# Kernel optimization log

Hardware: AMD Instinct MI355X
Metric: run time of the kernel (lower is better)

Reference implementation:

```python
import jax, jax.numpy as jnp
import numpy as np

BETA = 2
KERAS_EPS = 1e-7  # keras.backend.epsilon()


def _masks(n):
    idx = np.arange(n)
    # eps2[i,j] = 1 iff i<j  (itertools.combinations for N=2)
    eps2 = (idx[:, None] < idx[None, :]).astype(np.float32)
    # eps3[i,j,k] = 1 iff i<j<k  (itertools.combinations for N=3)
    eps3 = ((idx[:, None, None] < idx[None, :, None])
            & (idx[None, :, None] < idx[None, None, :])).astype(np.float32)
    return jnp.asarray(eps2), jnp.asarray(eps3)


def _jet_ecf(x, beta):
    # x: [B, n, 3] = (pt, eta, phi)
    n = x.shape[1]
    pt = x[:, :, 0]    # [B, n]
    eta = x[:, :, 1]
    phi = x[:, :, 2]
    # pairwise squared distance in (eta, phi): [B, n, n]
    R2 = (eta[:, :, None] - eta[:, None, :]) ** 2 \
       + (phi[:, :, None] - phi[:, None, :]) ** 2
    if beta == 2:
        Rb = R2
    elif beta == 1:
        Rb = jnp.sqrt(R2)
    else:
        Rb = R2 ** (beta / 2)

    eps2, eps3 = _masks(n)

    ecf1 = jnp.sum(pt, axis=-1, keepdims=True)                         # [B, 1]
    ecf2 = jnp.einsum('ij,ai,aj,aij->a', eps2, pt, pt, Rb)[:, None]    # [B, 1]
    ecf3 = jnp.einsum('ijk,ai,aj,ak,aij,aik,ajk->a',
                      eps3, pt, pt, pt, Rb, Rb, Rb)[:, None]           # [B, 1]
    return ecf1, ecf2, ecf3


def setup_inputs() -> dict:
    key = jax.random.key(0)
    x = jax.random.normal(key, (2048, 200, 3), dtype=jnp.float32)
    return {"x": x}


def reference(x):
    ecf1, ecf2, ecf3 = _jet_ecf(x, BETA)
    d2 = ecf3 * ecf1 ** 3 / (ecf2 ** 3 + KERAS_EPS)
    return jnp.concatenate([ecf1, ecf2, ecf3, d2], axis=-1)  # [B, 4]
```

## Files before the change

kernel.cpp:

```cpp
#include <hip/hip_runtime.h>


constexpr int NPART = 200;
typedef float f2 __attribute__((ext_vector_type(2)));

__device__ __forceinline__ float bcast(float v, int ii) {
    return __int_as_float(__builtin_amdgcn_readlane(__float_as_int(v), ii));
}

constexpr int offA(int g) {
    return (g < 72) ? g : (g == 135 ? 135 : g - 64);
}

struct Ctx {
    f2 bw[5], be[5], bp[5];
    f2 acc23, accY, tt;
    f2 pe01, pp01, pe23, pp23, pe13, pp13, n1;
    float a0, a1, a2, a3;
    float pe1, pp1, pe3, pp3;
    unsigned aw, ae, ap;
    int lane;
};

template <int G>
__device__ __forceinline__ void prefetch(Ctx& c) {
    constexpr int A = offA(G), B = G, S = G % 5;
    asm volatile(
        "ds_read2_b32 %[w], %[aw] offset0:%c[A] offset1:%c[B]\n\t"
        "ds_read2_b32 %[e], %[ae] offset0:%c[A] offset1:%c[B]\n\t"
        "ds_read2_b32 %[p], %[ap] offset0:%c[A] offset1:%c[B]\n\t"
        : [w] "+v"(c.bw[S]), [e] "+v"(c.be[S]), [p] "+v"(c.bp[S])
        : [aw] "v"(c.aw), [ae] "v"(c.ae), [ap] "v"(c.ap), [A] "i"(A), [B] "i"(B));
}

template <int G>
__device__ __forceinline__ void cstep(Ctx& c) {
    constexpr int rem = 198 - G;
    constexpr int K = 3 * (rem < 4 ? rem : 4);
    constexpr int S = G % 5;
    if constexpr (G <= 6) {
        f2 t1, t2;
        asm volatile(
            "s_waitcnt lgkmcnt(%c[K])\n\t"
            "v_pk_fma_f32 %[t1], %[pe01], %[n1], %[be]\n\t"
            "v_pk_fma_f32 %[t2], %[pp01], %[n1], %[bp]\n\t"
            "v_pk_mul_f32 %[t1], %[t1], %[t1]\n\t"
            "v_pk_mul_f32 %[t2], %[t2], %[t2]\n\t"
            "v_pk_add_f32 %[t1], %[t1], %[t2]\n\t"
            "v_pk_mul_f32 %[tt], %[t1], %[bw]\n\t"
            "v_pk_fma_f32 %[t1], %[pe23], %[n1], %[be]\n\t"
            "v_pk_fma_f32 %[t2], %[pp23], %[n1], %[bp]\n\t"
            "v_pk_mul_f32 %[t1], %[t1], %[t1]\n\t"
            "v_pk_mul_f32 %[t2], %[t2], %[t2]\n\t"
            "v_pk_add_f32 %[t1], %[t1], %[t2]\n\t"
            "v_pk_mul_f32 %[t1], %[t1], %[bw]\n\t"
            "v_pk_add_f32 %[acc], %[acc], %[t1]\n\t"
            : [t1] "=&v"(t1), [t2] "=&v"(t2), [tt] "=&v"(c.tt),
              [acc] "+v"(c.acc23), [bw] "+v"(c.bw[S]), [be] "+v"(c.be[S]),
              [bp] "+v"(c.bp[S])
            : [pe01] "v"(c.pe01), [pp01] "v"(c.pp01), [pe23] "v"(c.pe23),
              [pp23] "v"(c.pp23), [n1] "v"(c.n1), [K] "i"(K));
        c.a1 = __fadd_rn(c.a1, c.tt.y);
        c.a0 = __fadd_rn(c.a0, (G < c.lane) ? c.tt.x : 0.0f);
    } else if constexpr (G <= 71) {
        f2 t1, t2;
        asm volatile(
            "s_waitcnt lgkmcnt(%c[K])\n\t"
            "v_pk_fma_f32 %[t1], %[pe23], %[n1], %[be]\n\t"
            "v_pk_fma_f32 %[t2], %[pp23], %[n1], %[bp]\n\t"
            "v_pk_mul_f32 %[t1], %[t1], %[t1]\n\t"
            "v_pk_mul_f32 %[t2], %[t2], %[t2]\n\t"
            "v_pk_add_f32 %[t1], %[t1], %[t2]\n\t"
            "v_pk_mul_f32 %[t1], %[t1], %[bw]\n\t"
            "v_pk_add_f32 %[acc], %[acc], %[t1]\n\t"
            : [t1] "=&v"(t1), [t2] "=&v"(t2), [acc] "+v"(c.acc23),
              [bw] "+v"(c.bw[S]), [be] "+v"(c.be[S]), [bp] "+v"(c.bp[S])
            : [pe23] "v"(c.pe23), [pp23] "v"(c.pp23), [n1] "v"(c.n1), [K] "i"(K));
        if constexpr (G == 7) {
            const float de = __fsub_rn(c.be[S].x, c.pe1);
            const float dp = __fsub_rn(c.bp[S].x, c.pp1);
            const float r2 = __fadd_rn(__fmul_rn(de, de), __fmul_rn(dp, dp));
            c.a1 = __fadd_rn(c.a1, __fmul_rn(r2, c.bw[S].x));
        }
    } else if constexpr (G <= 134) {
        if constexpr (G == 72) { c.a2 = c.acc23.x; c.a3 = c.acc23.y; }
        f2 t1, t2;
        asm volatile(
            "s_waitcnt lgkmcnt(%c[K])\n\t"
            "v_pk_fma_f32 %[t1], %[pe13], %[n1], %[be]\n\t"
            "v_pk_fma_f32 %[t2], %[pp13], %[n1], %[bp]\n\t"
            "v_pk_mul_f32 %[t1], %[t1], %[t1]\n\t"
            "v_pk_mul_f32 %[t2], %[t2], %[t2]\n\t"
            "v_pk_add_f32 %[t1], %[t1], %[t2]\n\t"
            "v_pk_mul_f32 %[tt], %[t1], %[bw]\n\t"
            : [t1] "=&v"(t1), [t2] "=&v"(t2), [tt] "=&v"(c.tt),
              [bw] "+v"(c.bw[S]), [be] "+v"(c.be[S]), [bp] "+v"(c.bp[S])
            : [pe13] "v"(c.pe13), [pp13] "v"(c.pp13), [n1] "v"(c.n1), [K] "i"(K));
        c.a3 = __fadd_rn(c.a3, c.tt.y);
        c.a1 = __fadd_rn(c.a1, ((G - 72) < c.lane) ? c.tt.x : 0.0f);
    } else if constexpr (G == 135) {
        asm volatile("s_waitcnt lgkmcnt(%c[K])"
                     : [bw] "+v"(c.bw[S]), [be] "+v"(c.be[S]), [bp] "+v"(c.bp[S])
                     : [K] "i"(K));
        const float de = __fsub_rn(c.be[S].x, c.pe3);
        const float dp = __fsub_rn(c.bp[S].x, c.pp3);
        const float r2 = __fadd_rn(__fmul_rn(de, de), __fmul_rn(dp, dp));
        c.a3 = __fadd_rn(c.a3, __fmul_rn(r2, c.bw[S].x));
    } else {
        if constexpr (G == 136) { c.accY.x = c.a2; c.accY.y = c.a3; }
        constexpr unsigned sh = G - 135;
        constexpr unsigned lm = sh < 32 ? (0xFFFFFFFFu << sh) : 0u;
        constexpr unsigned hm = sh < 32 ? 0xFFFFFFFFu : (0xFFFFFFFFu << (sh - 32));
        f2 t1, t2;
        asm volatile(
            "s_waitcnt lgkmcnt(%c[K])\n\t"
            "s_mov_b32 exec_lo, %c[LM]\n\t"
            "s_mov_b32 exec_hi, %c[HM]\n\t"
            "v_pk_fma_f32 %[t1], %[pe23], %[n1], %[be]\n\t"
            "v_pk_fma_f32 %[t2], %[pp23], %[n1], %[bp]\n\t"
            "v_pk_mul_f32 %[t1], %[t1], %[t1]\n\t"
            "v_pk_mul_f32 %[t2], %[t2], %[t2]\n\t"
            "v_pk_add_f32 %[t1], %[t1], %[t2]\n\t"
            "v_pk_mul_f32 %[t1], %[t1], %[bw]\n\t"
            "v_pk_add_f32 %[acc], %[acc], %[t1]\n\t"
            "s_mov_b64 exec, -1\n\t"
            : [t1] "=&v"(t1), [t2] "=&v"(t2), [acc] "+v"(c.accY),
              [bw] "+v"(c.bw[S]), [be] "+v"(c.be[S]), [bp] "+v"(c.bp[S])
            : [pe23] "v"(c.pe23), [pp23] "v"(c.pp23), [n1] "v"(c.n1),
              [K] "i"(K), [LM] "i"(lm), [HM] "i"(hm));
    }
}

template <int G>
__device__ __forceinline__ void run(Ctx& c) {
    if constexpr (G <= 198) {
        cstep<G>(c);
        if constexpr (G + 5 <= 198) prefetch<G + 5>(c);
        run<G + 1>(c);
    }
}

__global__ __launch_bounds__(64) void jet_ecf_kernel(const float* __restrict__ x,
                                                     float* __restrict__ out,
                                                     int njet) {
#pragma clang fp contract(off)
    const int jet = blockIdx.x;
    if (jet >= njet) return;
    const int lane = threadIdx.x;
    const float* xj = x + (size_t)jet * NPART * 3;

    __shared__ float lds[600];

    float pw[4], pea[4], ppa[4];
    {
        const int base[4] = {0, 8, 72, 136};
        #pragma unroll
        for (int k = 0; k < 4; ++k) {
            const int p = base[k] + lane;
            const bool valid = (k > 0) || (lane < 8);
            if (valid) {
                pw[k] = xj[p * 3 + 0];
                pea[k] = xj[p * 3 + 1];
                ppa[k] = xj[p * 3 + 2];
            } else {
                pw[k] = 0.0f; pea[k] = 0.0f; ppa[k] = 0.0f;
            }
        }
    }

    #pragma unroll
    for (int r = 0; r < 4; ++r) {
        const int i = lane + (r << 6);
        if (i < NPART) {
            lds[i]       = xj[3 * i + 0];
            lds[200 + i] = xj[3 * i + 1];
            lds[400 + i] = xj[3 * i + 2];
        }
    }

    double S = 0, Sa = 0, Se = 0, Sp = 0, Saa = 0;
    double Sae = 0, Sap = 0, See = 0, Spp = 0, Sep = 0;
    #pragma unroll
    for (int k = 0; k < 4; ++k) {
        const double w = (double)pw[k];
        const double e = (double)pea[k];
        const double f = (double)ppa[k];
        const double a = e * e + f * f;
        S   += w;        Sa  += w * a;     Se  += w * e;
        Sp  += w * f;    Saa += w * a * a; Sae += w * a * e;
        Sap += w * a * f; See += w * e * e; Spp += w * f * f;
        Sep += w * e * f;
    }
    #pragma unroll
    for (int off = 32; off > 0; off >>= 1) {
        S   += __shfl_down(S,   off, 64);
        Sa  += __shfl_down(Sa,  off, 64);
        Se  += __shfl_down(Se,  off, 64);
        Sp  += __shfl_down(Sp,  off, 64);
        Saa += __shfl_down(Saa, off, 64);
        Sae += __shfl_down(Sae, off, 64);
        Sap += __shfl_down(Sap, off, 64);
        See += __shfl_down(See, off, 64);
        Spp += __shfl_down(Spp, off, 64);
        Sep += __shfl_down(Sep, off, 64);
    }

    __syncthreads();
    asm volatile("" ::: "memory");
    asm volatile("" :: "v"(S), "v"(Sa), "v"(Se), "v"(Sp), "v"(Saa),
                       "v"(Sae), "v"(Sap), "v"(See), "v"(Spp), "v"(Sep));
    __builtin_amdgcn_sched_barrier(0);
    asm volatile("s_waitcnt lgkmcnt(0)" ::: );

    Ctx c;
    c.lane = lane;
    c.aw = (unsigned)(uintptr_t)&lds[0];
    c.ae = (unsigned)(uintptr_t)&lds[200];
    c.ap = (unsigned)(uintptr_t)&lds[400];
    c.n1.x = -1.0f; c.n1.y = -1.0f;
    c.pe01.x = pea[0]; c.pe01.y = pea[1];
    c.pp01.x = ppa[0]; c.pp01.y = ppa[1];
    c.pe23.x = pea[2]; c.pe23.y = pea[3];
    c.pp23.x = ppa[2]; c.pp23.y = ppa[3];
    c.pe13.x = pea[1]; c.pe13.y = pea[3];
    c.pp13.x = ppa[1]; c.pp13.y = ppa[3];
    c.pe1 = pea[1]; c.pp1 = ppa[1]; c.pe3 = pea[3]; c.pp3 = ppa[3];
    c.acc23.x = 0.0f; c.acc23.y = 0.0f;
    c.accY.x = 0.0f;  c.accY.y = 0.0f;
    c.tt.x = 0.0f;    c.tt.y = 0.0f;
    c.a0 = c.a1 = c.a2 = c.a3 = 0.0f;
    #pragma unroll
    for (int k = 0; k < 5; ++k) {
        c.bw[k].x = 0.0f; c.bw[k].y = 0.0f;
        c.be[k].x = 0.0f; c.be[k].y = 0.0f;
        c.bp[k].x = 0.0f; c.bp[k].y = 0.0f;
    }

    prefetch<0>(c); prefetch<1>(c); prefetch<2>(c); prefetch<3>(c); prefetch<4>(c);
    run<0>(c);
    c.a2 = c.accY.x; c.a3 = c.accY.y;

    const float t0 = __fmul_rn(pw[0], c.a0);
    const float t1 = __fmul_rn(pw[1], c.a1);
    const float t2 = __fmul_rn(pw[2], c.a2);
    const float t3 = __fmul_rn(pw[3], c.a3);

    float e2f = 0.0f;
    #pragma unroll
    for (int ii = 0; ii < 8; ++ii)  e2f = __fadd_rn(e2f, bcast(t0, ii));
    #pragma unroll 8
    for (int ii = 0; ii < 64; ++ii) e2f = __fadd_rn(e2f, bcast(t1, ii));
    #pragma unroll 8
    for (int ii = 0; ii < 64; ++ii) e2f = __fadd_rn(e2f, bcast(t2, ii));
    #pragma unroll 8
    for (int ii = 0; ii < 64; ++ii) e2f = __fadd_rn(e2f, bcast(t3, ii));

    if (lane == 0) {
        const double A[4][4] = {
            {  Saa,        Sa,       -2.0 * Sae, -2.0 * Sap },
            {  Sa,         S,        -2.0 * Se,  -2.0 * Sp  },
            { -2.0 * Sae, -2.0 * Se,  4.0 * See,  4.0 * Sep },
            { -2.0 * Sap, -2.0 * Sp,  4.0 * Sep,  4.0 * Spp }
        };
        const double B[4][4] = {
            { Sa,  S,  -2.0 * Se,  -2.0 * Sp  },
            { Saa, Sa, -2.0 * Sae, -2.0 * Sap },
            { Sae, Se, -2.0 * See, -2.0 * Sep },
            { Sap, Sp, -2.0 * Sep, -2.0 * Spp }
        };
        const double C[4][4] = {
            { S,  Sa,  Se,  Sp  },
            { Sa, Saa, Sae, Sap },
            { Se, Sae, See, Sep },
            { Sp, Sap, Sep, Spp }
        };
        double T = 0.0;
        #pragma unroll
        for (int b = 0; b < 4; ++b) {
            #pragma unroll
            for (int g = 0; g < 4; ++g) {
                double ab = 0.0;
                #pragma unroll
                for (int al = 0; al < 4; ++al) ab += A[al][b] * B[al][g];
                T += ab * C[b][g];
            }
        }
        const double ecf1 = S;
        const double ecf2 = (double)e2f;
        const double ecf3 = T * (1.0 / 6.0);
        const double d2 = ecf3 * ecf1 * ecf1 * ecf1 / (ecf2 * ecf2 * ecf2 + 1e-7);
        float4 o = make_float4((float)ecf1, (float)ecf2, (float)ecf3, (float)d2);
        *reinterpret_cast<float4*>(out + (size_t)jet * 4) = o;
    }
}

extern "C" void kernel_launch(void* const* d_in, const int* in_sizes, int n_in,
                              void* d_out, int out_size, void* d_ws, size_t ws_size,
                              hipStream_t stream) {
    const float* x = (const float*)d_in[0];
    float* out = (float*)d_out;
    const int njet = in_sizes[0] / (NPART * 3);
    jet_ecf_kernel<<<njet, 64, 0, stream>>>(x, out, njet);
}
```

Baseline: 70.69 us.

## Replace readlane broadcast reduction with LDS staging and pack middle-phase accumulators

The final serial sum of 200 per-particle terms no longer uses 200 v_readlane broadcasts. Each term is written into a second shared array, partly early inside the main loop, and then read back as float4 vectors, keeping the sequential float add order. The middle phase now accumulates both outputs in one packed register pair with a cndmask lane mask instead of separate scalar adds. The moment sums use explicit double FMAs. The inline asm hardcodes v40-v43 and vcc as clobbers, and the LDS writes and reads are ordered only by a manual lgkmcnt wait with no barrier.

```diff
diff --git a/kernel.cpp b/kernel.cpp
--- a/kernel.cpp
+++ b/kernel.cpp
@@ -4,20 +4,18 @@
 constexpr int NPART = 200;
 typedef float f2 __attribute__((ext_vector_type(2)));
 
-__device__ __forceinline__ float bcast(float v, int ii) {
-    return __int_as_float(__builtin_amdgcn_readlane(__float_as_int(v), ii));
-}
-
 constexpr int offA(int g) {
     return (g < 72) ? g : (g == 135 ? 135 : g - 64);
 }
 
 struct Ctx {
     f2 bw[5], be[5], bp[5];
-    f2 acc23, accY, tt;
+    f2 acc23, accY, accM, tt;
     f2 pe01, pp01, pe23, pp23, pe13, pp13, n1;
-    float a0, a1, a2, a3;
+    float a0, a1;
     float pe1, pp1, pe3, pp3;
+    float pw0, pw1;
+    float* l2;
     unsigned aw, ae, ap;
     int lane;
 };
@@ -83,21 +81,23 @@
             c.a1 = __fadd_rn(c.a1, __fmul_rn(r2, c.bw[S].x));
         }
     } else if constexpr (G <= 134) {
-        if constexpr (G == 72) { c.a2 = c.acc23.x; c.a3 = c.acc23.y; }
-        f2 t1, t2;
+        if constexpr (G == 72) { c.accM.x = c.a1; c.accM.y = c.acc23.y; }
         asm volatile(
             "s_waitcnt lgkmcnt(%c[K])\n\t"
-            "v_pk_fma_f32 %[t1], %[pe13], %[n1], %[be]\n\t"
-            "v_pk_fma_f32 %[t2], %[pp13], %[n1], %[bp]\n\t"
-            "v_pk_mul_f32 %[t1], %[t1], %[t1]\n\t"
-            "v_pk_mul_f32 %[t2], %[t2], %[t2]\n\t"
-            "v_pk_add_f32 %[t1], %[t1], %[t2]\n\t"
-            "v_pk_mul_f32 %[tt], %[t1], %[bw]\n\t"
-            : [t1] "=&v"(t1), [t2] "=&v"(t2), [tt] "=&v"(c.tt),
-              [bw] "+v"(c.bw[S]), [be] "+v"(c.be[S]), [bp] "+v"(c.bp[S])
-            : [pe13] "v"(c.pe13), [pp13] "v"(c.pp13), [n1] "v"(c.n1), [K] "i"(K));
-        c.a3 = __fadd_rn(c.a3, c.tt.y);
-        c.a1 = __fadd_rn(c.a1, ((G - 72) < c.lane) ? c.tt.x : 0.0f);
+            "v_pk_fma_f32 v[40:41], %[pe13], %[n1], %[be]\n\t"
+            "v_pk_fma_f32 v[42:43], %[pp13], %[n1], %[bp]\n\t"
+            "v_pk_mul_f32 v[40:41], v[40:41], v[40:41]\n\t"
+            "v_pk_mul_f32 v[42:43], v[42:43], v[42:43]\n\t"
+            "v_pk_add_f32 v[40:41], v[40:41], v[42:43]\n\t"
+            "v_pk_mul_f32 v[40:41], v[40:41], %[bw]\n\t"
+            "v_cmp_lt_u32 vcc, %c[II], %[lane]\n\t"
+            "v_cndmask_b32 v40, 0, v40, vcc\n\t"
+            "v_pk_add_f32 %[acc], %[acc], v[40:41]\n\t"
+            : [acc] "+v"(c.accM), [bw] "+v"(c.bw[S]), [be] "+v"(c.be[S]),
+              [bp] "+v"(c.bp[S])
+            : [pe13] "v"(c.pe13), [pp13] "v"(c.pp13), [n1] "v"(c.n1),
+              [K] "i"(K), [II] "i"(G - 72), [lane] "v"(c.lane)
+            : "v40", "v41", "v42", "v43", "vcc");
     } else if constexpr (G == 135) {
         asm volatile("s_waitcnt lgkmcnt(%c[K])"
                      : [bw] "+v"(c.bw[S]), [be] "+v"(c.be[S]), [bp] "+v"(c.bp[S])
@@ -105,9 +105,9 @@
         const float de = __fsub_rn(c.be[S].x, c.pe3);
         const float dp = __fsub_rn(c.bp[S].x, c.pp3);
         const float r2 = __fadd_rn(__fmul_rn(de, de), __fmul_rn(dp, dp));
-        c.a3 = __fadd_rn(c.a3, __fmul_rn(r2, c.bw[S].x));
+        c.accM.y = __fadd_rn(c.accM.y, __fmul_rn(r2, c.bw[S].x));
     } else {
-        if constexpr (G == 136) { c.accY.x = c.a2; c.accY.y = c.a3; }
+        if constexpr (G == 136) { c.accY.x = c.acc23.x; c.accY.y = c.accM.y; }
         constexpr unsigned sh = G - 135;
         constexpr unsigned lm = sh < 32 ? (0xFFFFFFFFu << sh) : 0u;
         constexpr unsigned hm = sh < 32 ? 0xFFFFFFFFu : (0xFFFFFFFFu << (sh - 32));
@@ -135,6 +135,12 @@
 __device__ __forceinline__ void run(Ctx& c) {
     if constexpr (G <= 198) {
         cstep<G>(c);
+        if constexpr (G == 6) {
+            c.l2[c.lane] = __fmul_rn(c.pw0, c.a0);
+        }
+        if constexpr (G == 134) {
+            c.l2[8 + c.lane] = __fmul_rn(c.pw1, c.accM.x);
+        }
         if constexpr (G + 5 <= 198) prefetch<G + 5>(c);
         run<G + 1>(c);
     }
@@ -150,6 +156,7 @@
     const float* xj = x + (size_t)jet * NPART * 3;
 
     __shared__ float lds[600];
+    __shared__ __align__(16) float lds2[200];
 
     float pw[4], pea[4], ppa[4];
     {
@@ -185,11 +192,15 @@
         const double w = (double)pw[k];
         const double e = (double)pea[k];
         const double f = (double)ppa[k];
-        const double a = e * e + f * f;
-        S   += w;        Sa  += w * a;     Se  += w * e;
-        Sp  += w * f;    Saa += w * a * a; Sae += w * a * e;
-        Sap += w * a * f; See += w * e * e; Spp += w * f * f;
-        Sep += w * e * f;
+        const double a = fma(f, f, e * e);
+        const double wa = w * a, we = w * e, wf = w * f;
+        S += w; Sa += wa; Se += we; Sp += wf;
+        Saa = fma(wa, a, Saa);
+        Sae = fma(wa, e, Sae);
+        Sap = fma(wa, f, Sap);
+        See = fma(we, e, See);
+        Sep = fma(we, f, Sep);
+        Spp = fma(wf, f, Spp);
     }
     #pragma unroll
     for (int off = 32; off > 0; off >>= 1) {
@@ -217,6 +228,8 @@
     c.aw = (unsigned)(uintptr_t)&lds[0];
     c.ae = (unsigned)(uintptr_t)&lds[200];
     c.ap = (unsigned)(uintptr_t)&lds[400];
+    c.l2 = lds2;
+    c.pw0 = pw[0]; c.pw1 = pw[1];
     c.n1.x = -1.0f; c.n1.y = -1.0f;
     c.pe01.x = pea[0]; c.pe01.y = pea[1];
     c.pp01.x = ppa[0]; c.pp01.y = ppa[1];
@@ -227,8 +240,9 @@
     c.pe1 = pea[1]; c.pp1 = ppa[1]; c.pe3 = pea[3]; c.pp3 = ppa[3];
     c.acc23.x = 0.0f; c.acc23.y = 0.0f;
     c.accY.x = 0.0f;  c.accY.y = 0.0f;
+    c.accM.x = 0.0f;  c.accM.y = 0.0f;
     c.tt.x = 0.0f;    c.tt.y = 0.0f;
-    c.a0 = c.a1 = c.a2 = c.a3 = 0.0f;
+    c.a0 = c.a1 = 0.0f;
     #pragma unroll
     for (int k = 0; k < 5; ++k) {
         c.bw[k].x = 0.0f; c.bw[k].y = 0.0f;
@@ -238,22 +252,24 @@
 
     prefetch<0>(c); prefetch<1>(c); prefetch<2>(c); prefetch<3>(c); prefetch<4>(c);
     run<0>(c);
-    c.a2 = c.accY.x; c.a3 = c.accY.y;
-
-    const float t0 = __fmul_rn(pw[0], c.a0);
-    const float t1 = __fmul_rn(pw[1], c.a1);
-    const float t2 = __fmul_rn(pw[2], c.a2);
-    const float t3 = __fmul_rn(pw[3], c.a3);
+
+    lds2[72 + lane]  = __fmul_rn(pw[2], c.accY.x);
+    lds2[136 + lane] = __fmul_rn(pw[3], c.accY.y);
+
+    asm volatile("s_waitcnt lgkmcnt(0)" ::: "memory");
 
     float e2f = 0.0f;
-    #pragma unroll
-    for (int ii = 0; ii < 8; ++ii)  e2f = __fadd_rn(e2f, bcast(t0, ii));
-    #pragma unroll 8
-    for (int ii = 0; ii < 64; ++ii) e2f = __fadd_rn(e2f, bcast(t1, ii));
-    #pragma unroll 8
-    for (int ii = 0; ii < 64; ++ii) e2f = __fadd_rn(e2f, bcast(t2, ii));
-    #pragma unroll 8
-    for (int ii = 0; ii < 64; ++ii) e2f = __fadd_rn(e2f, bcast(t3, ii));
+    {
+        const float4* lt = reinterpret_cast<const float4*>(lds2);
+        #pragma unroll
+        for (int q = 0; q < 50; ++q) {
+            const float4 v = lt[q];
+            e2f = __fadd_rn(e2f, v.x);
+            e2f = __fadd_rn(e2f, v.y);
+            e2f = __fadd_rn(e2f, v.z);
+            e2f = __fadd_rn(e2f, v.w);
+        }
+    }
 
     if (lane == 0) {
         const double A[4][4] = {
```

Measured after the change: 69.70 us. Within noise of the previous version (-1.4%).
